# Performance work log

Hardware: AMD Instinct MI355X
Metric: run time of the kernel (lower is better)

## Reference

```python
import jax, jax.numpy as jnp
import numpy as np

N = 200000
D = 128
MAX_DEG = 12
BN_EPS = 1e-5


def setup_inputs() -> dict:
    key = jax.random.key(0)
    ks = jax.random.split(key, 8)
    s = 0.1
    feat = jax.random.normal(ks[0], (N, D), dtype=jnp.float32)
    W_ih = jax.random.normal(ks[1], (3 * D, D), dtype=jnp.float32) * s
    W_hh = jax.random.normal(ks[2], (3 * D, D), dtype=jnp.float32) * s
    b_ih = jax.random.normal(ks[3], (3 * D,), dtype=jnp.float32) * s
    b_hh = jax.random.normal(ks[4], (3 * D,), dtype=jnp.float32) * s
    W_self = jax.random.normal(ks[5], (D, D), dtype=jnp.float32) * s
    W_neigh = jax.random.normal(ks[6], (D, D), dtype=jnp.float32) * s
    gamma = jnp.ones((D,), dtype=jnp.float32)
    beta = jnp.zeros((D,), dtype=jnp.float32)
    # Ragged per-node mailboxes: random in-degree in [0, MAX_DEG], padded.
    rng = np.random.default_rng(0)
    deg = rng.integers(0, MAX_DEG + 1, size=N)
    src_idx = rng.integers(0, N, size=(N, MAX_DEG)).astype(np.int32)
    mask = (np.arange(MAX_DEG)[None, :] < deg[:, None])
    return {
        'feat': feat, 'gamma': gamma, 'beta': beta,
        'W_ih': W_ih, 'W_hh': W_hh, 'b_ih': b_ih, 'b_hh': b_hh,
        'W_self': W_self, 'W_neigh': W_neigh,
        'src_idx': jnp.asarray(src_idx), 'mask': jnp.asarray(mask),
    }


def _eopa_forward(feat, gamma, beta, W_ih, W_hh, b_ih, b_hh, W_self, W_neigh, src_idx, mask):
    # BatchNorm1d (training mode: batch statistics, biased variance)
    mu = jnp.mean(feat, axis=0)
    var = jnp.mean((feat - mu) ** 2, axis=0)
    x = (feat - mu) * jax.lax.rsqrt(var + BN_EPS) * gamma + beta  # [N, D]

    # Precompute input-gate projections are gathered per-step; scan over mailbox slots.
    def step(h, inp):
        src_t, m_t = inp            # [N] int, [N] bool
        xt = x[src_t]               # gather neighbor messages  [N, D]
        gi = xt @ W_ih.T + b_ih     # [N, 3D]
        gh = h @ W_hh.T + b_hh      # [N, 3D]
        ir, iz, inn = jnp.split(gi, 3, axis=1)
        hr, hz, hn = jnp.split(gh, 3, axis=1)
        r = jax.nn.sigmoid(ir + hr)
        z = jax.nn.sigmoid(iz + hz)
        n = jnp.tanh(inn + r * hn)
        h_new = (1.0 - z) * n + z * h
        # freeze hidden state past each node's true in-degree (ragged GRU)
        h = jnp.where(m_t[:, None], h_new, h)
        return h, None

    h0 = jnp.zeros_like(x)
    neigh, _ = jax.lax.scan(step, h0, (src_idx.T, mask.T))  # scan over MAX_DEG steps
    rst = x @ W_self.T + neigh @ W_neigh.T
    return rst


def reference(feat, gamma, beta, W_ih, W_hh, b_ih, b_hh, W_self, W_neigh, src_idx, mask):
    return _eopa_forward(feat, gamma, beta, W_ih, W_hh, b_ih, b_hh, W_self, W_neigh, src_idx, mask)
```

## Files before the change

kernel.cpp:

```cpp
#include <hip/hip_runtime.h>
#include <hip/hip_bf16.h>
#include <stdint.h>

#define NN 200000
#define DD 128

typedef __attribute__((ext_vector_type(8))) short short8;
typedef __attribute__((ext_vector_type(4))) float floatx4;

#define MFMA16(a,b,c) __builtin_amdgcn_mfma_f32_16x16x32_bf16(a,b,c,0,0,0)

static constexpr size_t WS_SUM    = 0;
static constexpr size_t WS_SQ     = 512;
static constexpr size_t WS_FLAG   = 1024;
static constexpr size_t WS_HIST   = 1088;
static constexpr size_t WS_OFF    = 1216;
static constexpr size_t WS_WHH    = 4096;
static constexpr size_t WS_WIH    = 102400;
static constexpr size_t WS_WSELF  = 200704;
static constexpr size_t WS_WNEIGH = 233472;
static constexpr size_t WS_DEG    = 266240;
static constexpr size_t WS_PERM   = 466240;
static constexpr size_t WS_XB     = 1266240;
static constexpr size_t WS_GI     = 52466240;

__device__ __forceinline__ uint16_t f2b(float f){
    uint32_t u = __builtin_bit_cast(uint32_t, f);
    uint32_t r = u + 0x7FFFu + ((u >> 16) & 1u);
    return (uint16_t)(r >> 16);
}
__device__ __forceinline__ float b2f(uint16_t h){
    uint32_t u = ((uint32_t)h) << 16;
    return __builtin_bit_cast(float, u);
}
__device__ __forceinline__ float sigm(float x){
    float e = __builtin_amdgcn_exp2f(x * -1.4426950408889634f);
    return __builtin_amdgcn_rcpf(1.0f + e);
}
__device__ __forceinline__ float tanh_(float x){
    float e = __builtin_amdgcn_exp2f(x * 2.8853900817779268f);
    return 1.0f - 2.0f * __builtin_amdgcn_rcpf(1.0f + e);
}

__global__ void k_init(float* __restrict__ ws){
    ws[threadIdx.x] = 0.0f;
    ws[threadIdx.x + 256] = 0.0f;
}

__global__ void k_detect(const uint32_t* __restrict__ mask_w, uint32_t* __restrict__ flag){
    __shared__ uint32_t any;
    if (threadIdx.x == 0) any = 0;
    __syncthreads();
    uint32_t loc = 0;
    for (int i = threadIdx.x; i < 4096; i += 256) loc |= (mask_w[i] & 0xFFFFFF00u);
    if (loc) atomicOr(&any, 1u);
    __syncthreads();
    if (threadIdx.x == 0) *flag = (any != 0) ? 1u : 0u;
}

__global__ void k_stats(const float* __restrict__ feat, float* __restrict__ wsum, float* __restrict__ wsq){
    __shared__ float ssum[256], ssq[256];
    const int col = threadIdx.x & 127, half = threadIdx.x >> 7;
    float s = 0.f, q = 0.f;
    for (int r = blockIdx.x * 2 + half; r < NN; r += gridDim.x * 2){
        float v = feat[(size_t)r * DD + col];
        s += v; q += v * v;
    }
    ssum[threadIdx.x] = s; ssq[threadIdx.x] = q;
    __syncthreads();
    if (threadIdx.x < 128){
        atomicAdd(&wsum[col], ssum[threadIdx.x] + ssum[threadIdx.x + 128]);
        atomicAdd(&wsq[col],  ssq[threadIdx.x]  + ssq[threadIdx.x + 128]);
    }
}

__global__ void k_prep(const float* __restrict__ Wih, const float* __restrict__ Whh,
                       const float* __restrict__ Wself, const float* __restrict__ Wneigh,
                       uint16_t* __restrict__ whh_c, uint16_t* __restrict__ wih_c,
                       uint16_t* __restrict__ wself_c, uint16_t* __restrict__ wneigh_c){
    int i = blockIdx.x * 256 + threadIdx.x;
    if (i < 49152){
        int j = i & 7, cidx = i >> 3, n = cidx % 384, kq = cidx / 384;
        whh_c[i] = f2b(Whh[n * 128 + kq * 8 + j]);
    } else if (i < 98304){
        int e = i - 49152;
        int j = e & 7, cidx = e >> 3, n = cidx % 384, kq = cidx / 384;
        wih_c[e] = f2b(Wih[n * 128 + kq * 8 + j]);
    } else if (i < 114688){
        int e = i - 98304;
        int j = e & 7, cidx = e >> 3, n = cidx & 127, kq = cidx >> 7;
        wself_c[e] = f2b(Wself[n * 128 + kq * 8 + j]);
    } else {
        int e = i - 114688;
        int j = e & 7, cidx = e >> 3, n = cidx & 127, kq = cidx >> 7;
        wneigh_c[e] = f2b(Wneigh[n * 128 + kq * 8 + j]);
    }
}

__global__ void k_hist(const void* __restrict__ mask, const uint32_t* __restrict__ flag,
                       uint8_t* __restrict__ deg, uint32_t* __restrict__ hist){
    __shared__ uint32_t lh[13];
    if (threadIdx.x < 13) lh[threadIdx.x] = 0;
    __syncthreads();
    const uint32_t flg = *flag;
    for (int n = blockIdx.x * 256 + threadIdx.x; n < NN; n += gridDim.x * 256){
        int d = 0;
        if (flg){
            const uint8_t* m = (const uint8_t*)mask + (size_t)n * 12;
            for (int t = 0; t < 12; t++) d += m[t] ? 1 : 0;
        } else {
            const int* m = (const int*)mask + (size_t)n * 12;
            for (int t = 0; t < 12; t++) d += m[t] ? 1 : 0;
        }
        deg[n] = (uint8_t)d;
        atomicAdd(&lh[d], 1u);
    }
    __syncthreads();
    if (threadIdx.x < 13 && lh[threadIdx.x]) atomicAdd(&hist[threadIdx.x], lh[threadIdx.x]);
}

__global__ void k_scan(const uint32_t* __restrict__ hist, uint32_t* __restrict__ off){
    if (threadIdx.x == 0){
        uint32_t acc = 0;
        for (int d = 12; d >= 0; d--){ off[d] = acc; acc += hist[d]; }
    }
}

__global__ void k_scatter(const uint8_t* __restrict__ deg, uint32_t* __restrict__ off,
                          int* __restrict__ perm){
    __shared__ uint32_t lh[13], basebuf[13];
    if (threadIdx.x < 13) lh[threadIdx.x] = 0;
    __syncthreads();
    int n = blockIdx.x * 256 + threadIdx.x;
    int d = 0; uint32_t r = 0;
    bool valid = n < NN;
    if (valid){ d = deg[n]; r = atomicAdd(&lh[d], 1u); }
    __syncthreads();
    if (threadIdx.x < 13 && lh[threadIdx.x]) basebuf[threadIdx.x] = atomicAdd(&off[threadIdx.x], lh[threadIdx.x]);
    __syncthreads();
    if (valid) perm[basebuf[d] + r] = n;
}

__global__ void k_bn(const float* __restrict__ feat, const float* __restrict__ gamma,
                     const float* __restrict__ beta, const float* __restrict__ wsum,
                     const float* __restrict__ wsq, uint16_t* __restrict__ xb){
    const int col = threadIdx.x & 127;
    const int strideRows = (gridDim.x * blockDim.x) >> 7;
    const int row0 = (blockIdx.x * blockDim.x + threadIdx.x) >> 7;
    float mu  = wsum[col] * (1.0f / NN);
    float var = wsq[col] * (1.0f / NN) - mu * mu;
    float rs  = rsqrtf(var + 1e-5f);
    float g = gamma[col] * rs;
    float b = beta[col] - mu * g;
    for (int r = row0; r < NN; r += strideRows)
        xb[(size_t)r * DD + col] = f2b(feat[(size_t)r * DD + col] * g + b);
}

__global__ __launch_bounds__(256) void k_gi(const uint16_t* __restrict__ xb,
                                            const uint16_t* __restrict__ wih_c,
                                            const float* __restrict__ b_ih,
                                            uint16_t* __restrict__ gi){
    const int tid = threadIdx.x, lane = tid & 63, w = tid >> 6, q = lane >> 4, c = lane & 15;
    const int wrow = (blockIdx.x * 4 + w) * 64;
    if (wrow >= NN) return;
    short8 A[4][4];
#pragma unroll
    for (int m = 0; m < 4; m++)
#pragma unroll
        for (int kb = 0; kb < 4; kb++)
            A[m][kb] = *(const short8*)(xb + (size_t)(wrow + m * 16 + c) * 128 + kb * 32 + q * 8);
#pragma unroll
    for (int nb = 0; nb < 24; nb++){
        floatx4 acc[4];
#pragma unroll
        for (int m = 0; m < 4; m++) acc[m] = floatx4{0.f, 0.f, 0.f, 0.f};
#pragma unroll
        for (int kb = 0; kb < 4; kb++){
            short8 B = *(const short8*)(wih_c + ((size_t)(kb * 4 + q) * 384 + nb * 16 + c) * 8);
#pragma unroll
            for (int m = 0; m < 4; m++) acc[m] = MFMA16(A[m][kb], B, acc[m]);
        }
        int colg = nb * 16 + c;
        float bias = b_ih[colg];
#pragma unroll
        for (int m = 0; m < 4; m++)
#pragma unroll
            for (int j = 0; j < 4; j++){
                int row = wrow + m * 16 + q * 4 + j;
                gi[(size_t)row * 384 + colg] = f2b(acc[m][j] + bias);
            }
    }
}

__global__ __launch_bounds__(256, 1) void k_gru(
    const uint16_t* __restrict__ xb, const uint16_t* __restrict__ gi,
    const uint16_t* __restrict__ whh_c, const uint16_t* __restrict__ wself_c,
    const uint16_t* __restrict__ wneigh_c, const float* __restrict__ b_hh,
    const int* __restrict__ src_idx, const void* __restrict__ mask,
    const uint32_t* __restrict__ flag, const int* __restrict__ perm,
    const uint8_t* __restrict__ degp, float* __restrict__ out)
{
    __shared__ __align__(16) uint16_t hbuf[2][64][136];
    __shared__ int src_s[768];
    __shared__ uint8_t mask_s[768];
    __shared__ int perm_s[64];
    __shared__ int tmax_s;

    const int tid = threadIdx.x, lane = tid & 63, w = tid >> 6, q = lane >> 4, c = lane & 15;
    const int base = blockIdx.x * 64;

    if (tid < 64) perm_s[tid] = perm[base + tid];
    if (tid == 0) tmax_s = 0;
    __syncthreads();

    const uint32_t flg = *flag;
    for (int i = tid; i < 768; i += 256){
        int node = perm_s[i / 12];
        size_t offn = (size_t)node * 12 + (i % 12);
        src_s[i] = src_idx[offn];
        uint8_t mv;
        if (flg) mv = ((const uint8_t*)mask)[offn] ? 1 : 0;
        else     mv = ((const int*)mask)[offn] ? 1 : 0;
        mask_s[i] = mv;
    }
    if (tid < 64) atomicMax(&tmax_s, (int)degp[perm_s[tid]]);
    for (int i = tid; i < 64 * 136 / 2; i += 256) ((uint32_t*)hbuf[0])[i] = 0;

    short8 Bh[3][2][4];
    float bhh[3][2];
#pragma unroll
    for (int g = 0; g < 3; g++)
#pragma unroll
        for (int p = 0; p < 2; p++){
            int n = g * 128 + w * 32 + p * 16 + c;
            bhh[g][p] = b_hh[n];
#pragma unroll
            for (int kb = 0; kb < 4; kb++)
                Bh[g][p][kb] = *(const short8*)(whh_c + ((size_t)(kb * 4 + q) * 384 + n) * 8);
        }

    float hC[4][2][4];
#pragma unroll
    for (int m = 0; m < 4; m++)
#pragma unroll
        for (int p = 0; p < 2; p++)
#pragma unroll
            for (int j = 0; j < 4; j++) hC[m][p][j] = 0.f;

    __syncthreads();
    const int tmax = tmax_s;

    for (int t = 0; t < tmax; t++){
        const int rb = t & 1, wbuf = rb ^ 1;
        uint16_t gv[4][3][2][4];
        uint8_t  mk[4][4];
#pragma unroll
        for (int m = 0; m < 4; m++)
#pragma unroll
            for (int j = 0; j < 4; j++){
                int row = m * 16 + q * 4 + j;
                int s = src_s[row * 12 + t];
                mk[m][j] = mask_s[row * 12 + t];
                const uint16_t* a = gi + (size_t)s * 384 + w * 32 + c;
                gv[m][0][0][j] = a[0];   gv[m][0][1][j] = a[16];
                gv[m][1][0][j] = a[128]; gv[m][1][1][j] = a[144];
                gv[m][2][0][j] = a[256]; gv[m][2][1][j] = a[272];
            }
#pragma unroll
        for (int m = 0; m < 4; m++){
            short8 A[4];
#pragma unroll
            for (int kb = 0; kb < 4; kb++)
                A[kb] = *(const short8*)&hbuf[rb][m * 16 + c][kb * 32 + q * 8];
            floatx4 acc[3][2];
#pragma unroll
            for (int g = 0; g < 3; g++)
#pragma unroll
                for (int p = 0; p < 2; p++){
                    floatx4 a0 = {0.f, 0.f, 0.f, 0.f};
#pragma unroll
                    for (int kb = 0; kb < 4; kb++) a0 = MFMA16(A[kb], Bh[g][p][kb], a0);
                    acc[g][p] = a0;
                }
#pragma unroll
            for (int p = 0; p < 2; p++)
#pragma unroll
                for (int j = 0; j < 4; j++){
                    float grv = b2f(gv[m][0][p][j]) + acc[0][p][j] + bhh[0][p];
                    float gzv = b2f(gv[m][1][p][j]) + acc[1][p][j] + bhh[1][p];
                    float hn  = acc[2][p][j] + bhh[2][p];
                    float r = sigm(grv);
                    float z = sigm(gzv);
                    float nn = tanh_(b2f(gv[m][2][p][j]) + r * hn);
                    float hold = hC[m][p][j];
                    float hnew = nn + z * (hold - nn);
                    hnew = mk[m][j] ? hnew : hold;
                    hC[m][p][j] = hnew;
                    hbuf[wbuf][m * 16 + q * 4 + j][w * 32 + p * 16 + c] = f2b(hnew);
                }
        }
        __syncthreads();
    }

    const int fb = tmax & 1;

    floatx4 acc2[4][2];
#pragma unroll
    for (int m = 0; m < 4; m++)
#pragma unroll
        for (int p = 0; p < 2; p++) acc2[m][p] = floatx4{0.f, 0.f, 0.f, 0.f};
#pragma unroll
    for (int m = 0; m < 4; m++){
        short8 A[4];
#pragma unroll
        for (int kb = 0; kb < 4; kb++)
            A[kb] = *(const short8*)&hbuf[fb][m * 16 + c][kb * 32 + q * 8];
#pragma unroll
        for (int p = 0; p < 2; p++)
#pragma unroll
            for (int kb = 0; kb < 4; kb++){
                short8 B = *(const short8*)(wneigh_c + ((size_t)(kb * 4 + q) * 128 + w * 32 + p * 16 + c) * 8);
                acc2[m][p] = MFMA16(A[kb], B, acc2[m][p]);
            }
    }
#pragma unroll
    for (int m = 0; m < 4; m++){
        int xrow = perm_s[m * 16 + c];
        short8 A[4];
#pragma unroll
        for (int kb = 0; kb < 4; kb++)
            A[kb] = *(const short8*)(xb + (size_t)xrow * 128 + kb * 32 + q * 8);
#pragma unroll
        for (int p = 0; p < 2; p++)
#pragma unroll
            for (int kb = 0; kb < 4; kb++){
                short8 B = *(const short8*)(wself_c + ((size_t)(kb * 4 + q) * 128 + w * 32 + p * 16 + c) * 8);
                acc2[m][p] = MFMA16(A[kb], B, acc2[m][p]);
            }
    }
#pragma unroll
    for (int m = 0; m < 4; m++){
#pragma unroll
        for (int j = 0; j < 4; j++){
            int orow = perm_s[m * 16 + q * 4 + j];
#pragma unroll
            for (int p = 0; p < 2; p++)
                out[(size_t)orow * 128 + w * 32 + p * 16 + c] = acc2[m][p][j];
        }
    }
}

extern "C" void kernel_launch(void* const* d_in, const int* in_sizes, int n_in,
                              void* d_out, int out_size, void* d_ws, size_t ws_size,
                              hipStream_t stream) {
    const float* feat    = (const float*)d_in[0];
    const float* gamma   = (const float*)d_in[1];
    const float* beta    = (const float*)d_in[2];
    const float* W_ih    = (const float*)d_in[3];
    const float* W_hh    = (const float*)d_in[4];
    const float* b_ih    = (const float*)d_in[5];
    const float* b_hh    = (const float*)d_in[6];
    const float* W_self  = (const float*)d_in[7];
    const float* W_neigh = (const float*)d_in[8];
    const int*   src_idx = (const int*)d_in[9];
    const void*  mask    = (const void*)d_in[10];
    float* out = (float*)d_out;

    char* ws = (char*)d_ws;
    float*    wsum     = (float*)(ws + WS_SUM);
    float*    wsq      = (float*)(ws + WS_SQ);
    uint32_t* flag     = (uint32_t*)(ws + WS_FLAG);
    uint32_t* hist     = (uint32_t*)(ws + WS_HIST);
    uint32_t* off      = (uint32_t*)(ws + WS_OFF);
    uint16_t* whh_c    = (uint16_t*)(ws + WS_WHH);
    uint16_t* wih_c    = (uint16_t*)(ws + WS_WIH);
    uint16_t* wself_c  = (uint16_t*)(ws + WS_WSELF);
    uint16_t* wneigh_c = (uint16_t*)(ws + WS_WNEIGH);
    uint8_t*  deg      = (uint8_t*)(ws + WS_DEG);
    int*      perm     = (int*)(ws + WS_PERM);
    uint16_t* xb       = (uint16_t*)(ws + WS_XB);
    uint16_t* gi       = (uint16_t*)(ws + WS_GI);

    k_init   <<<1,    256, 0, stream>>>((float*)ws);
    k_detect <<<1,    256, 0, stream>>>((const uint32_t*)mask, flag);
    k_stats  <<<512,  256, 0, stream>>>(feat, wsum, wsq);
    k_prep   <<<512,  256, 0, stream>>>(W_ih, W_hh, W_self, W_neigh, whh_c, wih_c, wself_c, wneigh_c);
    k_hist   <<<256,  256, 0, stream>>>(mask, flag, deg, hist);
    k_scan   <<<1,    64,  0, stream>>>(hist, off);
    k_scatter<<<782,  256, 0, stream>>>(deg, off, perm);
    k_bn     <<<782,  256, 0, stream>>>(feat, gamma, beta, wsum, wsq, xb);
    k_gi     <<<782,  256, 0, stream>>>(xb, wih_c, b_ih, gi);
    k_gru    <<<3125, 256, 0, stream>>>(xb, gi, whh_c, wself_c, wneigh_c, b_hh, src_idx, mask, flag, perm, deg, out);
}
```

Measured before the change: 778.7 us.

## Fuse input-gate GEMM into GRU kernel, widen blocks, vectorize stats and BN

Removes the separate k_gi pass that materialized a bf16 N×384 input-gate tensor. Instead, the GRU kernel gathers neighbor xb rows, prefetching the next step's rows, and computes the input projections with MFMA at every step. The GRU block grows to 512 threads, each wave owning 16 output columns with both weight sets held in registers, and the barrier becomes an explicit waitcnt plus s_barrier. The stats and BN kernels are vectorized with float4 loads, and stats atomics are spread over 8 replica slots to cut contention. The trade is more MFMA work per step and higher register pressure in exchange for avoiding the large gi write and its random reads.

```diff
diff --git a/kernel.cpp b/kernel.cpp
--- a/kernel.cpp
+++ b/kernel.cpp
@@ -11,18 +11,17 @@
 #define MFMA16(a,b,c) __builtin_amdgcn_mfma_f32_16x16x32_bf16(a,b,c,0,0,0)
 
 static constexpr size_t WS_SUM    = 0;
-static constexpr size_t WS_SQ     = 512;
-static constexpr size_t WS_FLAG   = 1024;
-static constexpr size_t WS_HIST   = 1088;
-static constexpr size_t WS_OFF    = 1216;
-static constexpr size_t WS_WHH    = 4096;
-static constexpr size_t WS_WIH    = 102400;
-static constexpr size_t WS_WSELF  = 200704;
-static constexpr size_t WS_WNEIGH = 233472;
-static constexpr size_t WS_DEG    = 266240;
-static constexpr size_t WS_PERM   = 466240;
-static constexpr size_t WS_XB     = 1266240;
-static constexpr size_t WS_GI     = 52466240;
+static constexpr size_t WS_SQ     = 4096;
+static constexpr size_t WS_FLAG   = 8192;
+static constexpr size_t WS_HIST   = 8256;
+static constexpr size_t WS_OFF    = 8384;
+static constexpr size_t WS_WHH    = 16384;
+static constexpr size_t WS_WIH    = 114688;
+static constexpr size_t WS_WSELF  = 212992;
+static constexpr size_t WS_WNEIGH = 245760;
+static constexpr size_t WS_DEG    = 278528;
+static constexpr size_t WS_PERM   = 478528;
+static constexpr size_t WS_XB     = 1278528;
 
 __device__ __forceinline__ uint16_t f2b(float f){
     uint32_t u = __builtin_bit_cast(uint32_t, f);
@@ -43,8 +42,8 @@
 }
 
 __global__ void k_init(float* __restrict__ ws){
-    ws[threadIdx.x] = 0.0f;
-    ws[threadIdx.x + 256] = 0.0f;
+#pragma unroll
+    for (int k = 0; k < 9; k++) ws[threadIdx.x + k * 256] = 0.0f;
 }
 
 __global__ void k_detect(const uint32_t* __restrict__ mask_w, uint32_t* __restrict__ flag){
@@ -59,18 +58,28 @@
 }
 
 __global__ void k_stats(const float* __restrict__ feat, float* __restrict__ wsum, float* __restrict__ wsq){
-    __shared__ float ssum[256], ssq[256];
-    const int col = threadIdx.x & 127, half = threadIdx.x >> 7;
-    float s = 0.f, q = 0.f;
-    for (int r = blockIdx.x * 2 + half; r < NN; r += gridDim.x * 2){
-        float v = feat[(size_t)r * DD + col];
-        s += v; q += v * v;
-    }
-    ssum[threadIdx.x] = s; ssq[threadIdx.x] = q;
-    __syncthreads();
-    if (threadIdx.x < 128){
-        atomicAdd(&wsum[col], ssum[threadIdx.x] + ssum[threadIdx.x + 128]);
-        atomicAdd(&wsq[col],  ssq[threadIdx.x]  + ssq[threadIdx.x + 128]);
+    __shared__ float rs_[256][5], rq_[256][5];
+    const int cg = threadIdx.x & 31, rr = threadIdx.x >> 5;
+    float s0=0,s1=0,s2=0,s3=0,q0=0,q1=0,q2=0,q3=0;
+    const float4* f4 = (const float4*)feat;
+    for (int r = blockIdx.x * 8 + rr; r < NN; r += gridDim.x * 8){
+        float4 v = f4[(size_t)r * 32 + cg];
+        s0+=v.x; s1+=v.y; s2+=v.z; s3+=v.w;
+        q0+=v.x*v.x; q1+=v.y*v.y; q2+=v.z*v.z; q3+=v.w*v.w;
+    }
+    rs_[threadIdx.x][0]=s0; rs_[threadIdx.x][1]=s1; rs_[threadIdx.x][2]=s2; rs_[threadIdx.x][3]=s3;
+    rq_[threadIdx.x][0]=q0; rq_[threadIdx.x][1]=q1; rq_[threadIdx.x][2]=q2; rq_[threadIdx.x][3]=q3;
+    __syncthreads();
+    if (threadIdx.x < 32){
+        const int rep = (blockIdx.x & 7) * 128;
+#pragma unroll
+        for (int k = 0; k < 4; k++){
+            float a = 0.f, b = 0.f;
+#pragma unroll
+            for (int r = 0; r < 8; r++){ a += rs_[r*32+threadIdx.x][k]; b += rq_[r*32+threadIdx.x][k]; }
+            atomicAdd(&wsum[rep + threadIdx.x*4 + k], a);
+            atomicAdd(&wsq [rep + threadIdx.x*4 + k], b);
+        }
     }
 }
 
@@ -144,58 +153,38 @@
 __global__ void k_bn(const float* __restrict__ feat, const float* __restrict__ gamma,
                      const float* __restrict__ beta, const float* __restrict__ wsum,
                      const float* __restrict__ wsq, uint16_t* __restrict__ xb){
-    const int col = threadIdx.x & 127;
-    const int strideRows = (gridDim.x * blockDim.x) >> 7;
-    const int row0 = (blockIdx.x * blockDim.x + threadIdx.x) >> 7;
-    float mu  = wsum[col] * (1.0f / NN);
-    float var = wsq[col] * (1.0f / NN) - mu * mu;
-    float rs  = rsqrtf(var + 1e-5f);
-    float g = gamma[col] * rs;
-    float b = beta[col] - mu * g;
-    for (int r = row0; r < NN; r += strideRows)
-        xb[(size_t)r * DD + col] = f2b(feat[(size_t)r * DD + col] * g + b);
-}
-
-__global__ __launch_bounds__(256) void k_gi(const uint16_t* __restrict__ xb,
-                                            const uint16_t* __restrict__ wih_c,
-                                            const float* __restrict__ b_ih,
-                                            uint16_t* __restrict__ gi){
-    const int tid = threadIdx.x, lane = tid & 63, w = tid >> 6, q = lane >> 4, c = lane & 15;
-    const int wrow = (blockIdx.x * 4 + w) * 64;
-    if (wrow >= NN) return;
-    short8 A[4][4];
-#pragma unroll
-    for (int m = 0; m < 4; m++)
-#pragma unroll
-        for (int kb = 0; kb < 4; kb++)
-            A[m][kb] = *(const short8*)(xb + (size_t)(wrow + m * 16 + c) * 128 + kb * 32 + q * 8);
-#pragma unroll
-    for (int nb = 0; nb < 24; nb++){
-        floatx4 acc[4];
-#pragma unroll
-        for (int m = 0; m < 4; m++) acc[m] = floatx4{0.f, 0.f, 0.f, 0.f};
-#pragma unroll
-        for (int kb = 0; kb < 4; kb++){
-            short8 B = *(const short8*)(wih_c + ((size_t)(kb * 4 + q) * 384 + nb * 16 + c) * 8);
-#pragma unroll
-            for (int m = 0; m < 4; m++) acc[m] = MFMA16(A[m][kb], B, acc[m]);
-        }
-        int colg = nb * 16 + c;
-        float bias = b_ih[colg];
-#pragma unroll
-        for (int m = 0; m < 4; m++)
-#pragma unroll
-            for (int j = 0; j < 4; j++){
-                int row = wrow + m * 16 + q * 4 + j;
-                gi[(size_t)row * 384 + colg] = f2b(acc[m][j] + bias);
-            }
-    }
-}
-
-__global__ __launch_bounds__(256, 1) void k_gru(
-    const uint16_t* __restrict__ xb, const uint16_t* __restrict__ gi,
-    const uint16_t* __restrict__ whh_c, const uint16_t* __restrict__ wself_c,
-    const uint16_t* __restrict__ wneigh_c, const float* __restrict__ b_hh,
+    const int c8 = (threadIdx.x & 15) * 8;
+    const int rr = threadIdx.x >> 4;
+    float g[8], b[8];
+#pragma unroll
+    for (int k = 0; k < 8; k++){
+        int col = c8 + k;
+        float su = 0.f, sq = 0.f;
+#pragma unroll
+        for (int r = 0; r < 8; r++){ su += wsum[r*128+col]; sq += wsq[r*128+col]; }
+        float mu  = su * (1.0f / NN);
+        float var = sq * (1.0f / NN) - mu * mu;
+        float rs  = rsqrtf(var + 1e-5f);
+        float gg  = gamma[col] * rs;
+        g[k] = gg; b[k] = beta[col] - mu * gg;
+    }
+    for (int r = blockIdx.x * 16 + rr; r < NN; r += gridDim.x * 16){
+        const float4* f4 = (const float4*)(feat + (size_t)r * 128 + c8);
+        float4 v0 = f4[0], v1 = f4[1];
+        short8 o;
+        o[0]=(short)f2b(v0.x*g[0]+b[0]); o[1]=(short)f2b(v0.y*g[1]+b[1]);
+        o[2]=(short)f2b(v0.z*g[2]+b[2]); o[3]=(short)f2b(v0.w*g[3]+b[3]);
+        o[4]=(short)f2b(v1.x*g[4]+b[4]); o[5]=(short)f2b(v1.y*g[5]+b[5]);
+        o[6]=(short)f2b(v1.z*g[6]+b[6]); o[7]=(short)f2b(v1.w*g[7]+b[7]);
+        *(short8*)(xb + (size_t)r * 128 + c8) = o;
+    }
+}
+
+__global__ __launch_bounds__(512, 2) void k_gru(
+    const uint16_t* __restrict__ xb,
+    const uint16_t* __restrict__ whh_c, const uint16_t* __restrict__ wih_c,
+    const uint16_t* __restrict__ wself_c, const uint16_t* __restrict__ wneigh_c,
+    const float* __restrict__ b_ih, const float* __restrict__ b_hh,
     const int* __restrict__ src_idx, const void* __restrict__ mask,
     const uint32_t* __restrict__ flag, const int* __restrict__ perm,
     const uint8_t* __restrict__ degp, float* __restrict__ out)
@@ -214,7 +203,7 @@
     __syncthreads();
 
     const uint32_t flg = *flag;
-    for (int i = tid; i < 768; i += 256){
+    for (int i = tid; i < 768; i += 512){
         int node = perm_s[i / 12];
         size_t offn = (size_t)node * 12 + (i % 12);
         src_s[i] = src_idx[offn];
@@ -224,91 +213,100 @@
         mask_s[i] = mv;
     }
     if (tid < 64) atomicMax(&tmax_s, (int)degp[perm_s[tid]]);
-    for (int i = tid; i < 64 * 136 / 2; i += 256) ((uint32_t*)hbuf[0])[i] = 0;
-
-    short8 Bh[3][2][4];
-    float bhh[3][2];
-#pragma unroll
-    for (int g = 0; g < 3; g++)
-#pragma unroll
-        for (int p = 0; p < 2; p++){
-            int n = g * 128 + w * 32 + p * 16 + c;
-            bhh[g][p] = b_hh[n];
-#pragma unroll
-            for (int kb = 0; kb < 4; kb++)
-                Bh[g][p][kb] = *(const short8*)(whh_c + ((size_t)(kb * 4 + q) * 384 + n) * 8);
-        }
-
-    float hC[4][2][4];
+    for (int i = tid; i < 64 * 136 * 2 / 4; i += 512) ((uint32_t*)hbuf[0])[i] = 0;
+
+    short8 Bi[3][4], Bh[3][4];
+    float bs0, bs1, bi2, bh2;
+    {
+        const int n0 = w * 16 + c;
+#pragma unroll
+        for (int g = 0; g < 3; g++){
+            int n = g * 128 + n0;
+#pragma unroll
+            for (int kb = 0; kb < 4; kb++){
+                Bi[g][kb] = *(const short8*)(wih_c + ((size_t)(kb * 4 + q) * 384 + n) * 8);
+                Bh[g][kb] = *(const short8*)(whh_c + ((size_t)(kb * 4 + q) * 384 + n) * 8);
+            }
+        }
+        bs0 = b_ih[n0]       + b_hh[n0];
+        bs1 = b_ih[128 + n0] + b_hh[128 + n0];
+        bi2 = b_ih[256 + n0];
+        bh2 = b_hh[256 + n0];
+    }
+
+    float hC[4][4];
 #pragma unroll
     for (int m = 0; m < 4; m++)
 #pragma unroll
-        for (int p = 0; p < 2; p++)
-#pragma unroll
-            for (int j = 0; j < 4; j++) hC[m][p][j] = 0.f;
+        for (int j = 0; j < 4; j++) hC[m][j] = 0.f;
 
     __syncthreads();
     const int tmax = tmax_s;
 
-    for (int t = 0; t < tmax; t++){
-        const int rb = t & 1, wbuf = rb ^ 1;
-        uint16_t gv[4][3][2][4];
-        uint8_t  mk[4][4];
-#pragma unroll
-        for (int m = 0; m < 4; m++)
-#pragma unroll
-            for (int j = 0; j < 4; j++){
-                int row = m * 16 + q * 4 + j;
-                int s = src_s[row * 12 + t];
-                mk[m][j] = mask_s[row * 12 + t];
-                const uint16_t* a = gi + (size_t)s * 384 + w * 32 + c;
-                gv[m][0][0][j] = a[0];   gv[m][0][1][j] = a[16];
-                gv[m][1][0][j] = a[128]; gv[m][1][1][j] = a[144];
-                gv[m][2][0][j] = a[256]; gv[m][2][1][j] = a[272];
+    if (tmax > 0){
+        short8 Ax[4][4];
+#pragma unroll
+        for (int m = 0; m < 4; m++){
+            int s = src_s[(m * 16 + c) * 12];
+            const uint16_t* a = xb + (size_t)s * 128 + q * 8;
+#pragma unroll
+            for (int kb = 0; kb < 4; kb++) Ax[m][kb] = *(const short8*)(a + kb * 32);
+        }
+        for (int t = 0; t < tmax; t++){
+            const int rb = t & 1, wbuf = rb ^ 1;
+            const int tn = (t + 1 < tmax) ? t + 1 : t;
+#pragma unroll
+            for (int m = 0; m < 4; m++){
+                short8 Ah[4];
+#pragma unroll
+                for (int kb = 0; kb < 4; kb++)
+                    Ah[kb] = *(const short8*)&hbuf[rb][m * 16 + c][kb * 32 + q * 8];
+                floatx4 agi[3], agh[3];
+#pragma unroll
+                for (int g = 0; g < 3; g++){
+                    floatx4 x0 = {0.f, 0.f, 0.f, 0.f}, h0 = {0.f, 0.f, 0.f, 0.f};
+#pragma unroll
+                    for (int kb = 0; kb < 4; kb++){
+                        x0 = MFMA16(Ax[m][kb], Bi[g][kb], x0);
+                        h0 = MFMA16(Ah[kb],    Bh[g][kb], h0);
+                    }
+                    agi[g] = x0; agh[g] = h0;
+                }
+                {
+                    int s = src_s[(m * 16 + c) * 12 + tn];
+                    const uint16_t* a = xb + (size_t)s * 128 + q * 8;
+#pragma unroll
+                    for (int kb = 0; kb < 4; kb++) Ax[m][kb] = *(const short8*)(a + kb * 32);
+                }
+#pragma unroll
+                for (int j = 0; j < 4; j++){
+                    uint8_t mk = mask_s[(m * 16 + q * 4 + j) * 12 + t];
+                    float r  = sigm(agi[0][j] + agh[0][j] + bs0);
+                    float z  = sigm(agi[1][j] + agh[1][j] + bs1);
+                    float hn = agh[2][j] + bh2;
+                    float nn = tanh_(agi[2][j] + bi2 + r * hn);
+                    float hold = hC[m][j];
+                    float hnew = nn + z * (hold - nn);
+                    hnew = mk ? hnew : hold;
+                    hC[m][j] = hnew;
+                    hbuf[wbuf][m * 16 + q * 4 + j][w * 16 + c] = f2b(hnew);
+                }
             }
-#pragma unroll
-        for (int m = 0; m < 4; m++){
-            short8 A[4];
-#pragma unroll
-            for (int kb = 0; kb < 4; kb++)
-                A[kb] = *(const short8*)&hbuf[rb][m * 16 + c][kb * 32 + q * 8];
-            floatx4 acc[3][2];
-#pragma unroll
-            for (int g = 0; g < 3; g++)
-#pragma unroll
-                for (int p = 0; p < 2; p++){
-                    floatx4 a0 = {0.f, 0.f, 0.f, 0.f};
-#pragma unroll
-                    for (int kb = 0; kb < 4; kb++) a0 = MFMA16(A[kb], Bh[g][p][kb], a0);
-                    acc[g][p] = a0;
-                }
-#pragma unroll
-            for (int p = 0; p < 2; p++)
-#pragma unroll
-                for (int j = 0; j < 4; j++){
-                    float grv = b2f(gv[m][0][p][j]) + acc[0][p][j] + bhh[0][p];
-                    float gzv = b2f(gv[m][1][p][j]) + acc[1][p][j] + bhh[1][p];
-                    float hn  = acc[2][p][j] + bhh[2][p];
-                    float r = sigm(grv);
-                    float z = sigm(gzv);
-                    float nn = tanh_(b2f(gv[m][2][p][j]) + r * hn);
-                    float hold = hC[m][p][j];
-                    float hnew = nn + z * (hold - nn);
-                    hnew = mk[m][j] ? hnew : hold;
-                    hC[m][p][j] = hnew;
-                    hbuf[wbuf][m * 16 + q * 4 + j][w * 32 + p * 16 + c] = f2b(hnew);
-                }
-        }
-        __syncthreads();
+            asm volatile("s_waitcnt lgkmcnt(0)\n\ts_barrier" ::: "memory");
+        }
     }
 
     const int fb = tmax & 1;
 
-    floatx4 acc2[4][2];
-#pragma unroll
-    for (int m = 0; m < 4; m++)
-#pragma unroll
-        for (int p = 0; p < 2; p++) acc2[m][p] = floatx4{0.f, 0.f, 0.f, 0.f};
+    floatx4 acc2[4];
+#pragma unroll
+    for (int m = 0; m < 4; m++) acc2[m] = floatx4{0.f, 0.f, 0.f, 0.f};
+    short8 Bs_[4], Bn_[4];
+#pragma unroll
+    for (int kb = 0; kb < 4; kb++){
+        Bs_[kb] = *(const short8*)(wself_c  + ((size_t)(kb * 4 + q) * 128 + w * 16 + c) * 8);
+        Bn_[kb] = *(const short8*)(wneigh_c + ((size_t)(kb * 4 + q) * 128 + w * 16 + c) * 8);
+    }
 #pragma unroll
     for (int m = 0; m < 4; m++){
         short8 A[4];
@@ -316,36 +314,20 @@
         for (int kb = 0; kb < 4; kb++)
             A[kb] = *(const short8*)&hbuf[fb][m * 16 + c][kb * 32 + q * 8];
 #pragma unroll
-        for (int p = 0; p < 2; p++)
-#pragma unroll
-            for (int kb = 0; kb < 4; kb++){
-                short8 B = *(const short8*)(wneigh_c + ((size_t)(kb * 4 + q) * 128 + w * 32 + p * 16 + c) * 8);
-                acc2[m][p] = MFMA16(A[kb], B, acc2[m][p]);
-            }
-    }
-#pragma unroll
-    for (int m = 0; m < 4; m++){
+        for (int kb = 0; kb < 4; kb++) acc2[m] = MFMA16(A[kb], Bn_[kb], acc2[m]);
         int xrow = perm_s[m * 16 + c];
-        short8 A[4];
-#pragma unroll
-        for (int kb = 0; kb < 4; kb++)
-            A[kb] = *(const short8*)(xb + (size_t)xrow * 128 + kb * 32 + q * 8);
-#pragma unroll
-        for (int p = 0; p < 2; p++)
-#pragma unroll
-            for (int kb = 0; kb < 4; kb++){
-                short8 B = *(const short8*)(wself_c + ((size_t)(kb * 4 + q) * 128 + w * 32 + p * 16 + c) * 8);
-                acc2[m][p] = MFMA16(A[kb], B, acc2[m][p]);
-            }
+        const uint16_t* a = xb + (size_t)xrow * 128 + q * 8;
+#pragma unroll
+        for (int kb = 0; kb < 4; kb++) A[kb] = *(const short8*)(a + kb * 32);
+#pragma unroll
+        for (int kb = 0; kb < 4; kb++) acc2[m] = MFMA16(A[kb], Bs_[kb], acc2[m]);
     }
 #pragma unroll
     for (int m = 0; m < 4; m++){
 #pragma unroll
         for (int j = 0; j < 4; j++){
             int orow = perm_s[m * 16 + q * 4 + j];
-#pragma unroll
-            for (int p = 0; p < 2; p++)
-                out[(size_t)orow * 128 + w * 32 + p * 16 + c] = acc2[m][p][j];
+            out[(size_t)orow * 128 + w * 16 + c] = acc2[m][j];
         }
     }
 }
@@ -379,7 +361,6 @@
     uint8_t*  deg      = (uint8_t*)(ws + WS_DEG);
     int*      perm     = (int*)(ws + WS_PERM);
     uint16_t* xb       = (uint16_t*)(ws + WS_XB);
-    uint16_t* gi       = (uint16_t*)(ws + WS_GI);
 
     k_init   <<<1,    256, 0, stream>>>((float*)ws);
     k_detect <<<1,    256, 0, stream>>>((const uint32_t*)mask, flag);
@@ -389,6 +370,6 @@
     k_scan   <<<1,    64,  0, stream>>>(hist, off);
     k_scatter<<<782,  256, 0, stream>>>(deg, off, perm);
     k_bn     <<<782,  256, 0, stream>>>(feat, gamma, beta, wsum, wsq, xb);
-    k_gi     <<<782,  256, 0, stream>>>(xb, wih_c, b_ih, gi);
-    k_gru    <<<3125, 256, 0, stream>>>(xb, gi, whh_c, wself_c, wneigh_c, b_hh, src_idx, mask, flag, perm, deg, out);
-}
+    k_gru    <<<3125, 512, 0, stream>>>(xb, whh_c, wih_c, wself_c, wneigh_c, b_ih, b_hh,
+                                        src_idx, mask, flag, perm, deg, out);
+}
```

Result: faster. 755.6 us (-3.0%).
